# Kernel optimization log

Measured on AMD Instinct MI355X. Metric: run time of the kernel, lower is better.

## Reference

```python
import math
import jax, jax.numpy as jnp
import numpy as np

N_HEADS = 32
N_KV_HEADS = 8
HEAD_DIM = 64
DIM = 2048
BATCH = 1
SEQ = 2048


def setup_inputs() -> dict:
    key = jax.random.key(0)
    ks = jax.random.split(key, 7)
    x = jax.random.normal(ks[0], (BATCH, SEQ, DIM), dtype=jnp.float32)
    # RoPE frequencies, llama2.c style: [seq_len, head_dim//2]
    inv_freq = 1.0 / (10000.0 ** (np.arange(0, HEAD_DIM, 2, dtype=np.float32) / HEAD_DIM))
    t = np.arange(SEQ, dtype=np.float32)
    freqs = np.outer(t, inv_freq)  # [SEQ, HEAD_DIM//2]
    freqs_cos = jnp.asarray(np.cos(freqs), dtype=jnp.float32)
    freqs_sin = jnp.asarray(np.sin(freqs), dtype=jnp.float32)
    s = 0.02
    wq = jax.random.normal(ks[1], (N_HEADS * HEAD_DIM, DIM), dtype=jnp.float32) * s
    wk = jax.random.normal(ks[2], (N_KV_HEADS * HEAD_DIM, DIM), dtype=jnp.float32) * s
    wv = jax.random.normal(ks[3], (N_KV_HEADS * HEAD_DIM, DIM), dtype=jnp.float32) * s
    wo = jax.random.normal(ks[4], (DIM, N_HEADS * HEAD_DIM), dtype=jnp.float32) * s
    return {"x": x, "freqs_cos": freqs_cos, "freqs_sin": freqs_sin,
            "wq": wq, "wk": wk, "wv": wv, "wo": wo}


def _apply_rotary(q, k, cos, sin):
    # q: [B,S,H,D], k: [B,S,Hkv,D]; cos/sin: [S, D//2]
    def rot(t):
        tr = t[..., 0::2]  # real parts (even lanes)
        ti = t[..., 1::2]  # imag parts (odd lanes)
        c = cos[None, :, None, :]
        s = sin[None, :, None, :]
        out_r = tr * c - ti * s
        out_i = tr * s + ti * c
        # re-interleave
        return jnp.stack([out_r, out_i], axis=-1).reshape(t.shape)
    return rot(q), rot(k)


def reference(x, freqs_cos, freqs_sin, wq, wk, wv, wo):
    B, S, _ = x.shape
    n_rep = N_HEADS // N_KV_HEADS
    xq = (x @ wq.T).reshape(B, S, N_HEADS, HEAD_DIM)
    xk = (x @ wk.T).reshape(B, S, N_KV_HEADS, HEAD_DIM)
    xv = (x @ wv.T).reshape(B, S, N_KV_HEADS, HEAD_DIM)
    xq, xk = _apply_rotary(xq, xk, freqs_cos, freqs_sin)
    # repeat_kv: [B,S,Hkv,D] -> [B,S,Hkv*n_rep,D]
    xk = jnp.repeat(xk, n_rep, axis=2)
    xv = jnp.repeat(xv, n_rep, axis=2)
    # [B,H,S,D]
    q = xq.transpose(0, 2, 1, 3)
    k = xk.transpose(0, 2, 1, 3)
    v = xv.transpose(0, 2, 1, 3)
    scores = jnp.einsum('bhqd,bhkd->bhqk', q, k) / math.sqrt(HEAD_DIM)
    causal = jnp.triu(jnp.ones((S, S), dtype=bool), k=1)
    scores = jnp.where(causal[None, None], -jnp.inf, scores)
    weights = jax.nn.softmax(scores, axis=-1)
    out = jnp.einsum('bhqk,bhkd->bhqd', weights, v)
    out = out.transpose(0, 2, 1, 3).reshape(B, S, N_HEADS * HEAD_DIM)
    return out @ wo.T
```

## Files before the change

### kernel.cpp

```cpp
#include <hip/hip_runtime.h>
#include <hip/hip_bf16.h>

#define DIM 2048
#define SEQ 2048
#define HD 64
#define NH 32
#define NKV 8

typedef __bf16 bf16x8 __attribute__((ext_vector_type(8)));
typedef __bf16 bf16x4 __attribute__((ext_vector_type(4)));
typedef float f32x4 __attribute__((ext_vector_type(4)));
typedef float f32x16 __attribute__((ext_vector_type(16)));
typedef unsigned short ushortx8 __attribute__((ext_vector_type(8)));
typedef unsigned short ushortx4 __attribute__((ext_vector_type(4)));
typedef unsigned short ushort_t;

#define QSCALE 0.1803368801111f

#define CHUNK 8
#define SLOTS_PER_H 40

__device__ __forceinline__ float hexp2(float x) {
    return __builtin_amdgcn_exp2f(x);
}

__device__ __forceinline__ unsigned short f2bf(float f) {
    unsigned int u = __builtin_bit_cast(unsigned int, f);
    u = (u + 0x7FFFu + ((u >> 16) & 1u)) >> 16;
    return (unsigned short)u;
}
__device__ __forceinline__ float bf2f(unsigned short h) {
    return __builtin_bit_cast(float, (unsigned int)h << 16);
}

__device__ __forceinline__ f32x4 mfma16(bf16x8 a, bf16x8 b, f32x4 c) {
    return __builtin_amdgcn_mfma_f32_16x16x32_bf16(a, b, c, 0, 0, 0);
}
__device__ __forceinline__ f32x16 mfma32(bf16x8 a, bf16x8 b, f32x16 c) {
    return __builtin_amdgcn_mfma_f32_32x32x16_bf16(a, b, c, 0, 0, 0);
}

__device__ __forceinline__ void gload16(const ushort_t* g, ushort_t* l) {
    __builtin_amdgcn_global_load_lds(
        (const __attribute__((address_space(1))) unsigned int*)g,
        (__attribute__((address_space(3))) unsigned int*)l, 16, 0, 0);
}

#define NX  (SEQ * DIM)
#define NWQ (DIM * DIM)
#define NWK (NKV * HD * DIM)
#define NWO (DIM * NH * HD)

__global__ __launch_bounds__(256)
void cvt5(const float* __restrict__ x, const float* __restrict__ wq,
          const float* __restrict__ wk, const float* __restrict__ wv,
          const float* __restrict__ wo,
          ushort_t* __restrict__ xb, ushort_t* __restrict__ wqb,
          ushort_t* __restrict__ wkb, ushort_t* __restrict__ wvb,
          ushort_t* __restrict__ wob)
{
    const int S0 = NX / 4, S1 = S0 + NWQ / 4, S2 = S1 + NWK / 4,
              S3 = S2 + NWK / 4, S4 = S3 + NWO / 4;
    for (int g = blockIdx.x * blockDim.x + threadIdx.x; g < S4;
         g += gridDim.x * blockDim.x) {
        const float* src; ushort_t* dst; int off;
        if (g < S0)      { src = x;  dst = xb;  off = g; }
        else if (g < S1) { src = wq; dst = wqb; off = g - S0; }
        else if (g < S2) { src = wk; dst = wkb; off = g - S1; }
        else if (g < S3) { src = wv; dst = wvb; off = g - S2; }
        else             { src = wo; dst = wob; off = g - S3; }
        float4 v = ((const float4*)src)[off];
        ushortx4 h = { f2bf(v.x), f2bf(v.y), f2bf(v.z), f2bf(v.w) };
        ((ushortx4*)dst)[off] = h;
    }
}

__global__ __launch_bounds__(256)
void qkv_rope(const ushort_t* __restrict__ xb,
              const ushort_t* __restrict__ wqb, const ushort_t* __restrict__ wkb,
              const ushort_t* __restrict__ wvb,
              ushort_t* __restrict__ Qb, ushort_t* __restrict__ Kb,
              ushort_t* __restrict__ VtG,
              const float* __restrict__ cosp, const float* __restrict__ sinp)
{
    __shared__ ushort_t As[2][128 * 64];
    __shared__ ushort_t Bs[2][64 * 64];

    const int nt = blockIdx.x;
    const ushort_t* Bw; int bn0; int seg;
    if (nt < 32)      { seg = 0; Bw = wqb; bn0 = nt * 64; }
    else if (nt < 40) { seg = 1; Bw = wkb; bn0 = (nt - 32) * 64; }
    else              { seg = 2; Bw = wvb; bn0 = (nt - 40) * 64; }

    const int tid  = threadIdx.x;
    const int lane = tid & 63;
    const int wid  = tid >> 6;
    const int wr = wid >> 1, wc = wid & 1;
    const int bm0 = blockIdx.y * 128;
    const int g16 = lane >> 4, l16 = lane & 15;
    const int sr  = tid >> 3;
    const int scb = (tid & 7) * 16;
    const int scsw = (scb ^ ((sr & 7) << 4)) >> 1;
    const int xorb = (l16 & 7) << 4;

    f32x4 acc[4][2] = {};

    auto STAGE = [&](int k0, int b) {
#pragma unroll
        for (int i = 0; i < 4; i++) {
            int r = sr + i * 32;
            gload16(xb + (size_t)(bm0 + r) * DIM + k0 + scsw, &As[b][(i * 256 + tid) * 8]);
        }
#pragma unroll
        for (int i = 0; i < 2; i++) {
            int r = sr + i * 32;
            gload16(Bw + (size_t)(bn0 + r) * DIM + k0 + scsw, &Bs[b][(i * 256 + tid) * 8]);
        }
    };

    STAGE(0, 0);

    for (int k0 = 0; k0 < DIM; k0 += 64) {
        const int b = (k0 >> 6) & 1;
        __syncthreads();
        if (k0 + 64 < DIM) STAGE(k0 + 64, b ^ 1);
#pragma unroll
        for (int kk = 0; kk < 2; kk++) {
            const int ci = ((kk * 64 + g16 * 16) ^ xorb) >> 1;
            bf16x8 af[4], bfr[2];
#pragma unroll
            for (int mi = 0; mi < 4; mi++)
                af[mi] = *(const bf16x8*)&As[b][(wr * 64 + mi * 16 + l16) * 64 + ci];
#pragma unroll
            for (int ni = 0; ni < 2; ni++)
                bfr[ni] = *(const bf16x8*)&Bs[b][(wc * 32 + ni * 16 + l16) * 64 + ci];
#pragma unroll
            for (int mi = 0; mi < 4; mi++)
#pragma unroll
                for (int ni = 0; ni < 2; ni++)
                    acc[mi][ni] = mfma16(af[mi], bfr[ni], acc[mi][ni]);
        }
    }

#pragma unroll
    for (int mi = 0; mi < 4; mi++) {
#pragma unroll
        for (int ni = 0; ni < 2; ni++) {
            const int row0 = bm0 + wr * 64 + mi * 16 + g16 * 4;
            const int col  = bn0 + wc * 32 + ni * 16 + l16;
            f32x4 v = acc[mi][ni];
            if (seg <= 1) {
                ushort_t* C = (seg == 0) ? Qb : Kb;
                const int ldC = (seg == 0) ? NH * HD : NKV * HD;
                const int d   = col & (HD - 1);
                const int p   = d >> 1;
                const bool odd = d & 1;
#pragma unroll
                for (int r = 0; r < 4; r++) {
                    float val = v[r];
                    float partner = __shfl_xor(val, 1);
                    int m = row0 + r;
                    float c = cosp[m * (HD / 2) + p];
                    float s = sinp[m * (HD / 2) + p];
                    float o = odd ? (partner * s + val * c) : (val * c - partner * s);
                    if (seg == 0) o *= QSCALE;
                    C[(size_t)m * ldC + col] = f2bf(o);
                }
            } else {
                const int pg = ((g16 & 1) << 1) | (g16 >> 1);
                const int rowp = bm0 + wr * 64 + mi * 16 + pg * 4;
                ushortx4 hv = { f2bf(v[0]), f2bf(v[1]), f2bf(v[2]), f2bf(v[3]) };
                *(ushortx4*)&VtG[(size_t)col * SEQ + rowp] = hv;
            }
        }
    }
}

__global__ __launch_bounds__(256)
void attn_fwd(const ushort_t* __restrict__ Q,
              const ushort_t* __restrict__ K,
              const ushort_t* __restrict__ VtG,
              ushort_t* __restrict__ Opart, float* __restrict__ Lpart,
              ushort_t* __restrict__ Ab)
{
    __shared__ ushort_t Ks[2][64 * 64];
    __shared__ ushort_t Vt[2][64 * 64];

    const int h  = blockIdx.x;
    const int kh = h >> 2;
    int y = blockIdx.y, qi = 0, pref = 0;
    for (;;) {
        int nch = (2 * qi + 9) >> 3;
        if (y < nch) break;
        y -= nch; pref += nch; qi++;
    }
    const int c = y;
    const int nchq = (2 * qi + 9) >> 3;
    const int kt0 = c * CHUNK;
    const int ktN = min(kt0 + CHUNK, 2 * qi + 2);
    const int sidx = h * SLOTS_PER_H + pref + c;

    const int tid = threadIdx.x;
    const int lane = tid & 63;
    const int w = tid >> 6;
    const int l32 = lane & 31;
    const int hi  = lane >> 5;
    const int sr = tid >> 3;
    const int scb = (tid & 7) * 16;
    const int scsw = (scb ^ ((sr & 7) << 4)) >> 1;
    const int rx = (l32 & 7) << 4;

    const int qw = qi * 128 + w * 32;

    bf16x8 qf[4];
#pragma unroll
    for (int ds = 0; ds < 4; ds++)
        qf[ds] = *(const bf16x8*)&Q[(size_t)(qw + l32) * (NH * HD) + h * HD + ds * 16 + hi * 8];

    f32x16 accO0 = {}, accO1 = {};
    float lsum = 0.f;

    auto STAGE = [&](int kt, int bf) {
#pragma unroll
        for (int i = 0; i < 2; i++) {
            int row = sr + i * 32;
            gload16(K   + (size_t)(kt * 64 + row) * (NKV * HD) + kh * HD + scsw,
                    &Ks[bf][(i * 256 + tid) * 8]);
            gload16(VtG + (size_t)(kh * HD + row) * SEQ + kt * 64 + scsw,
                    &Vt[bf][(i * 256 + tid) * 8]);
        }
    };

    STAGE(kt0, 0);

    for (int kj = kt0; kj < ktN; kj++) {
        const int b = (kj - kt0) & 1;
        const int kb = kj * 64;
        __syncthreads();
        if (kj + 1 < ktN) STAGE(kj + 1, b ^ 1);

        if (kb <= qw + 31) {
            f32x16 s0 = {}, s1 = {};
            __builtin_amdgcn_s_setprio(1);
#pragma unroll
            for (int ds = 0; ds < 4; ds++) {
                const int ci = (((32 * ds + 16 * hi)) ^ rx) >> 1;
                bf16x8 kf0 = *(const bf16x8*)&Ks[b][(l32)      * 64 + ci];
                bf16x8 kf1 = *(const bf16x8*)&Ks[b][(32 + l32) * 64 + ci];
                s0 = mfma32(kf0, qf[ds], s0);
                s1 = mfma32(kf1, qf[ds], s1);
            }
            __builtin_amdgcn_s_setprio(0);

            if (kb + 63 > qw) {
                const int qg = qw + l32;
#pragma unroll
                for (int r = 0; r < 16; r++) {
                    const int kl = (r & 3) + 8 * (r >> 2) + 4 * hi;
                    if (kb + kl > qg)      s0[r] = -1e30f;
                    if (kb + 32 + kl > qg) s1[r] = -1e30f;
                }
            }

            float p0[16], p1[16];
#pragma unroll
            for (int r = 0; r < 16; r++) { p0[r] = hexp2(s0[r]); p1[r] = hexp2(s1[r]); }
#pragma unroll
            for (int r = 0; r < 16; r++) lsum += p0[r] + p1[r];
            bf16x8 pa00, pa01, pa10, pa11;
#pragma unroll
            for (int e = 0; e < 8; e++) {
                pa00[e] = (__bf16)p0[e];  pa01[e] = (__bf16)p0[8 + e];
                pa10[e] = (__bf16)p1[e];  pa11[e] = (__bf16)p1[8 + e];
            }

            __builtin_amdgcn_s_setprio(1);
#pragma unroll
            for (int s = 0; s < 4; s++) {
                bf16x8 pa = (s == 0) ? pa00 : (s == 1) ? pa01 : (s == 2) ? pa10 : pa11;
                const int ci = (((32 * s + 16 * hi)) ^ rx) >> 1;
                bf16x8 vf0 = *(const bf16x8*)&Vt[b][(l32)      * 64 + ci];
                bf16x8 vf1 = *(const bf16x8*)&Vt[b][(32 + l32) * 64 + ci];
                accO0 = mfma32(pa, vf0, accO0);
                accO1 = mfma32(pa, vf1, accO1);
            }
            __builtin_amdgcn_s_setprio(0);
        }
    }

    lsum += __shfl_xor(lsum, 32);

    if (nchq == 1) {
#pragma unroll
        for (int r = 0; r < 16; r++) {
            const int qr = (r & 3) + 8 * (r >> 2) + 4 * hi;
            float ls = __shfl(lsum, qr);
            float inv = 1.0f / ls;
            size_t base = (size_t)(qw + qr) * (NH * HD) + h * HD;
            Ab[base + l32]      = f2bf(accO0[r] * inv);
            Ab[base + 32 + l32] = f2bf(accO1[r] * inv);
        }
    } else {
        ushort_t* op = Opart + (size_t)sidx * (128 * 64);
#pragma unroll
        for (int r = 0; r < 16; r++) {
            const int qr = (r & 3) + 8 * (r >> 2) + 4 * hi;
            ushort_t* rowp = op + (size_t)(w * 32 + qr) * 64;
            rowp[l32]      = f2bf(accO0[r]);
            rowp[32 + l32] = f2bf(accO1[r]);
        }
        if (hi == 0) Lpart[sidx * 128 + w * 32 + l32] = lsum;
    }
}

__global__ __launch_bounds__(256)
void attn_reduce(const ushort_t* __restrict__ Opart, const float* __restrict__ Lpart,
                 ushort_t* __restrict__ Ab)
{
    const int gid = blockIdx.x * 256 + threadIdx.x;
    const int g = gid & 7;
    const int h = (gid >> 3) & 31;
    const int m = gid >> 8;
    const int qi = m >> 7, rr = m & 127;
    if (qi < 4) return;
    int pref = 0;
#pragma unroll
    for (int q = 0; q < 16; q++) pref += (q < qi) ? ((2 * q + 9) >> 3) : 0;
    const int nch = (2 * qi + 9) >> 3;
    const int sbase = h * SLOTS_PER_H + pref;

    float sa[8] = {};
    float l = 0.f;
    for (int c = 0; c < nch; c++) {
        const ushort_t* rowp = Opart + ((size_t)(sbase + c) * 128 + rr) * 64 + g * 8;
        ushortx8 v = *(const ushortx8*)rowp;
#pragma unroll
        for (int e = 0; e < 8; e++) sa[e] += bf2f(v[e]);
        l += Lpart[(sbase + c) * 128 + rr];
    }
    const float inv = 1.0f / l;
    ushortx8 o;
#pragma unroll
    for (int e = 0; e < 8; e++) o[e] = f2bf(sa[e] * inv);
    *(ushortx8*)&Ab[(size_t)m * (NH * HD) + h * 64 + g * 8] = o;
}

__global__ __launch_bounds__(256)
void gemm_out(const ushort_t* __restrict__ A, const ushort_t* __restrict__ Bw,
              float* __restrict__ C)
{
    __shared__ ushort_t As[2][128 * 64];
    __shared__ ushort_t Bs[2][64 * 64];

    const int tid  = threadIdx.x;
    const int lane = tid & 63;
    const int wid  = tid >> 6;
    const int wr = wid >> 1, wc = wid & 1;
    const int bm0 = blockIdx.y * 128, bn0 = blockIdx.x * 64;
    const int g16 = lane >> 4, l16 = lane & 15;
    const int sr  = tid >> 3;
    const int scb = (tid & 7) * 16;
    const int scsw = (scb ^ ((sr & 7) << 4)) >> 1;
    const int xorb = (l16 & 7) << 4;

    f32x4 acc[4][2] = {};

    auto STAGE = [&](int k0, int b) {
#pragma unroll
        for (int i = 0; i < 4; i++) {
            int r = sr + i * 32;
            gload16(A + (size_t)(bm0 + r) * DIM + k0 + scsw, &As[b][(i * 256 + tid) * 8]);
        }
#pragma unroll
        for (int i = 0; i < 2; i++) {
            int r = sr + i * 32;
            gload16(Bw + (size_t)(bn0 + r) * DIM + k0 + scsw, &Bs[b][(i * 256 + tid) * 8]);
        }
    };

    STAGE(0, 0);

    for (int k0 = 0; k0 < DIM; k0 += 64) {
        const int b = (k0 >> 6) & 1;
        __syncthreads();
        if (k0 + 64 < DIM) STAGE(k0 + 64, b ^ 1);
#pragma unroll
        for (int kk = 0; kk < 2; kk++) {
            const int ci = ((kk * 64 + g16 * 16) ^ xorb) >> 1;
            bf16x8 af[4], bfr[2];
#pragma unroll
            for (int mi = 0; mi < 4; mi++)
                af[mi] = *(const bf16x8*)&As[b][(wr * 64 + mi * 16 + l16) * 64 + ci];
#pragma unroll
            for (int ni = 0; ni < 2; ni++)
                bfr[ni] = *(const bf16x8*)&Bs[b][(wc * 32 + ni * 16 + l16) * 64 + ci];
#pragma unroll
            for (int mi = 0; mi < 4; mi++)
#pragma unroll
                for (int ni = 0; ni < 2; ni++)
                    acc[mi][ni] = mfma16(af[mi], bfr[ni], acc[mi][ni]);
        }
    }

#pragma unroll
    for (int mi = 0; mi < 4; mi++) {
#pragma unroll
        for (int ni = 0; ni < 2; ni++) {
            const int row0 = bm0 + wr * 64 + mi * 16 + g16 * 4;
            const int col  = bn0 + wc * 32 + ni * 16 + l16;
#pragma unroll
            for (int r = 0; r < 4; r++)
                C[(size_t)(row0 + r) * DIM + col] = acc[mi][ni][r];
        }
    }
}

extern "C" void kernel_launch(void* const* d_in, const int* in_sizes, int n_in,
                              void* d_out, int out_size, void* d_ws, size_t ws_size,
                              hipStream_t stream)
{
    (void)in_sizes; (void)n_in; (void)out_size; (void)ws_size;
    const float* x    = (const float*)d_in[0];
    const float* fcos = (const float*)d_in[1];
    const float* fsin = (const float*)d_in[2];
    const float* wq   = (const float*)d_in[3];
    const float* wk   = (const float*)d_in[4];
    const float* wv   = (const float*)d_in[5];
    const float* wo   = (const float*)d_in[6];
    float* out = (float*)d_out;

    char* ws = (char*)d_ws;
    size_t off = 0;
    ushort_t* xb  = (ushort_t*)(ws + off); off += (size_t)NX  * 2;
    ushort_t* wqb = (ushort_t*)(ws + off); off += (size_t)NWQ * 2;
    ushort_t* wkb = (ushort_t*)(ws + off); off += (size_t)NWK * 2;
    ushort_t* wvb = (ushort_t*)(ws + off); off += (size_t)NWK * 2;
    ushort_t* wob = (ushort_t*)(ws + off); off += (size_t)NWO * 2;
    ushort_t* Qb  = (ushort_t*)(ws + off); off += (size_t)SEQ * NH * HD * 2;
    ushort_t* Kb  = (ushort_t*)(ws + off); off += (size_t)SEQ * NKV * HD * 2;
    ushort_t* VtG = (ushort_t*)(ws + off); off += (size_t)SEQ * NKV * HD * 2;
    ushort_t* Ab  = (ushort_t*)(ws + off); off += (size_t)SEQ * NH * HD * 2;
    ushort_t* Opart = (ushort_t*)(ws + off); off += (size_t)32 * SLOTS_PER_H * 128 * 64 * 2;
    float* Lpart  = (float*)(ws + off);      off += (size_t)32 * SLOTS_PER_H * 128 * 4;

    dim3 blk(256);
    cvt5<<<dim3(2048), blk, 0, stream>>>(x, wq, wk, wv, wo, xb, wqb, wkb, wvb, wob);
    qkv_rope<<<dim3(48, 16), blk, 0, stream>>>(xb, wqb, wkb, wvb, Qb, Kb, VtG, fcos, fsin);
    attn_fwd<<<dim3(32, SLOTS_PER_H), blk, 0, stream>>>(Qb, Kb, VtG, Opart, Lpart, Ab);
    attn_reduce<<<dim3(2048), blk, 0, stream>>>(Opart, Lpart, Ab);
    gemm_out<<<dim3(32, 16), blk, 0, stream>>>(Ab, wob, out);
}
```

Measured before the change: 123.6 us.

## Fuse split-K attention reduction into attn_fwd via atomic ticket last-block combine

Drops the separate attn_reduce kernel. Each attention block that writes a partial result now takes an atomic ticket per (head, query tile), and the last block to arrive sums the partial O and L values and writes the normalized output. This saves one kernel launch and the global round trip of a separate reduction pass. In exchange it adds a memset, threadfences and an atomic per block, and the final combine runs serially inside one block.

```diff
diff --git a/kernel.cpp b/kernel.cpp
--- a/kernel.cpp
+++ b/kernel.cpp
@@ -181,10 +181,11 @@
               const ushort_t* __restrict__ K,
               const ushort_t* __restrict__ VtG,
               ushort_t* __restrict__ Opart, float* __restrict__ Lpart,
-              ushort_t* __restrict__ Ab)
+              ushort_t* __restrict__ Ab, int* __restrict__ ticket)
 {
     __shared__ ushort_t Ks[2][64 * 64];
     __shared__ ushort_t Vt[2][64 * 64];
+    __shared__ int lastflag;
 
     const int h  = blockIdx.x;
     const int kh = h >> 2;
@@ -198,7 +199,8 @@
     const int nchq = (2 * qi + 9) >> 3;
     const int kt0 = c * CHUNK;
     const int ktN = min(kt0 + CHUNK, 2 * qi + 2);
-    const int sidx = h * SLOTS_PER_H + pref + c;
+    const int sbase0 = h * SLOTS_PER_H + pref;
+    const int sidx = sbase0 + c;
 
     const int tid = threadIdx.x;
     const int lane = tid & 63;
@@ -300,7 +302,10 @@
             Ab[base + l32]      = f2bf(accO0[r] * inv);
             Ab[base + 32 + l32] = f2bf(accO1[r] * inv);
         }
-    } else {
+        return;
+    }
+
+    {
         ushort_t* op = Opart + (size_t)sidx * (128 * 64);
 #pragma unroll
         for (int r = 0; r < 16; r++) {
@@ -311,38 +316,39 @@
         }
         if (hi == 0) Lpart[sidx * 128 + w * 32 + l32] = lsum;
     }
-}
-
-__global__ __launch_bounds__(256)
-void attn_reduce(const ushort_t* __restrict__ Opart, const float* __restrict__ Lpart,
-                 ushort_t* __restrict__ Ab)
-{
-    const int gid = blockIdx.x * 256 + threadIdx.x;
-    const int g = gid & 7;
-    const int h = (gid >> 3) & 31;
-    const int m = gid >> 8;
-    const int qi = m >> 7, rr = m & 127;
-    if (qi < 4) return;
-    int pref = 0;
-#pragma unroll
-    for (int q = 0; q < 16; q++) pref += (q < qi) ? ((2 * q + 9) >> 3) : 0;
-    const int nch = (2 * qi + 9) >> 3;
-    const int sbase = h * SLOTS_PER_H + pref;
-
-    float sa[8] = {};
-    float l = 0.f;
-    for (int c = 0; c < nch; c++) {
-        const ushort_t* rowp = Opart + ((size_t)(sbase + c) * 128 + rr) * 64 + g * 8;
-        ushortx8 v = *(const ushortx8*)rowp;
-#pragma unroll
-        for (int e = 0; e < 8; e++) sa[e] += bf2f(v[e]);
-        l += Lpart[(sbase + c) * 128 + rr];
-    }
-    const float inv = 1.0f / l;
-    ushortx8 o;
-#pragma unroll
-    for (int e = 0; e < 8; e++) o[e] = f2bf(sa[e] * inv);
-    *(ushortx8*)&Ab[(size_t)m * (NH * HD) + h * 64 + g * 8] = o;
+    __threadfence();
+    __syncthreads();
+    if (tid == 0) {
+        int old = atomicAdd(&ticket[h * 16 + qi], 1);
+        lastflag = (old == nchq - 1);
+    }
+    __syncthreads();
+    if (!lastflag) return;
+    __threadfence();
+
+    {
+        const int rr = tid >> 1;
+        const int c0 = (tid & 1) * 32;
+        float l = 0.f;
+        for (int c2 = 0; c2 < nchq; c2++)
+            l += Lpart[(sbase0 + c2) * 128 + rr];
+        const float inv = 1.0f / l;
+#pragma unroll
+        for (int s8 = 0; s8 < 4; s8++) {
+            float sa[8] = {};
+            for (int c2 = 0; c2 < nchq; c2++) {
+                const ushort_t* rowp =
+                    Opart + ((size_t)(sbase0 + c2) * 128 + rr) * 64 + c0 + s8 * 8;
+                ushortx8 v = *(const ushortx8*)rowp;
+#pragma unroll
+                for (int e = 0; e < 8; e++) sa[e] += bf2f(v[e]);
+            }
+            ushortx8 o;
+#pragma unroll
+            for (int e = 0; e < 8; e++) o[e] = f2bf(sa[e] * inv);
+            *(ushortx8*)&Ab[(size_t)(qi * 128 + rr) * (NH * HD) + h * 64 + c0 + s8 * 8] = o;
+        }
+    }
 }
 
 __global__ __launch_bounds__(256)
@@ -442,11 +448,13 @@
     ushort_t* Ab  = (ushort_t*)(ws + off); off += (size_t)SEQ * NH * HD * 2;
     ushort_t* Opart = (ushort_t*)(ws + off); off += (size_t)32 * SLOTS_PER_H * 128 * 64 * 2;
     float* Lpart  = (float*)(ws + off);      off += (size_t)32 * SLOTS_PER_H * 128 * 4;
+    int* ticket   = (int*)(ws + off);        off += (size_t)32 * 16 * 4;
+
+    hipMemsetAsync(ticket, 0, 32 * 16 * 4, stream);
 
     dim3 blk(256);
     cvt5<<<dim3(2048), blk, 0, stream>>>(x, wq, wk, wv, wo, xb, wqb, wkb, wvb, wob);
     qkv_rope<<<dim3(48, 16), blk, 0, stream>>>(xb, wqb, wkb, wvb, Qb, Kb, VtG, fcos, fsin);
-    attn_fwd<<<dim3(32, SLOTS_PER_H), blk, 0, stream>>>(Qb, Kb, VtG, Opart, Lpart, Ab);
-    attn_reduce<<<dim3(2048), blk, 0, stream>>>(Opart, Lpart, Ab);
+    attn_fwd<<<dim3(32, SLOTS_PER_H), blk, 0, stream>>>(Qb, Kb, VtG, Opart, Lpart, Ab, ticket);
     gemm_out<<<dim3(32, 16), blk, 0, stream>>>(Ab, wob, out);
 }
```

Result: slower. 312.0 us (+152.4%).
